# Kernel optimization log

Hardware: AMD Instinct MI355X
Metric: run time of the kernel (lower is better)

The kernel has to match this reference:

```python
import jax, jax.numpy as jnp
import numpy as np
from jax import lax

B, N, T = 64, 50, 30          # batch, history length, words per title
VOCAB, E = 50000, 300          # vocab size, word emb dim
FN, A, G, K = 400, 200, 400, 3 # filter_num, attention_dim, gru_unit, window size
USERS = 50000


def setup_inputs() -> dict:
    key = jax.random.key(0)
    ks = jax.random.split(key, 12)
    return {
        "user_id": jax.random.randint(ks[0], (B,), 0, USERS),
        "history_title": jax.random.randint(ks[1], (B, N, T), 0, VOCAB),
        "history_length": jax.random.randint(ks[2], (B,), 1, N + 1),
        "word_emb": jax.random.normal(ks[3], (VOCAB, E), jnp.float32) * 0.02,
        "conv_w": jax.random.normal(ks[4], (K, E, FN), jnp.float32) * 0.05,  # WIO layout
        "conv_b": jnp.zeros((FN,), jnp.float32),
        "v": jax.random.normal(ks[5], (FN, A), jnp.float32) * 0.05,
        "vb": jnp.zeros((A,), jnp.float32),
        "q": jax.random.normal(ks[6], (A, 1), jnp.float32) * 0.05,
        "user_emb": jax.random.normal(ks[7], (USERS, G), jnp.float32) * 0.02,
        "W_ih": jax.random.normal(ks[8], (3 * G, FN), jnp.float32) * 0.05,
        "W_hh": jax.random.normal(ks[9], (3 * G, G), jnp.float32) * 0.05,
        "b_ih": jnp.zeros((3 * G,), jnp.float32),
        "b_hh": jnp.zeros((3 * G,), jnp.float32),
    }


def _news_encode(history_title, word_emb, conv_w, conv_b, v, vb, q):
    # word embedding lookup: [B, N, T, E] (dropout is identity in eval mode)
    W = word_emb[history_title]
    # Conv1d over the word axis, padding=1 keeps length T
    x = W.reshape(B * N, T, E)
    C = lax.conv_general_dilated(
        x, conv_w, window_strides=(1,), padding=[(1, 1)],
        dimension_numbers=("NWC", "WIO", "NWC")) + conv_b
    C = jax.nn.relu(C).reshape(B, N, T, FN)
    # additive attention scores
    a = jnp.tanh(jnp.einsum("bntf,fa->bnta", C, v) + vb)
    a = jnp.einsum("bnta,ao->bnt", a, q)  # q: [A,1] -> squeeze
    # original uses Softmax(dim=0) on a [n, t] per sample => over the n-titles axis
    alpha = jax.nn.softmax(a, axis=1)
    # e[i] = alpha[i] @ C[i]: weighted sum over words -> [B, N, FN]
    return jnp.einsum("bnt,bntf->bnf", alpha, C)


def _gru(news_embed, h0, lengths, W_ih, W_hh, b_ih, b_hh):
    # packed_padded semantics: h stops updating once step >= length
    xs = jnp.swapaxes(news_embed, 0, 1)                 # [N, B, FN]
    mask = jnp.arange(N)[:, None] < lengths[None, :]    # [N, B]

    def step(h, inp):
        x_t, m = inp
        gx = x_t @ W_ih.T + b_ih                        # [B, 3G]
        gh = h @ W_hh.T + b_hh
        xr, xz, xn = jnp.split(gx, 3, axis=-1)
        hr, hz, hn = jnp.split(gh, 3, axis=-1)
        r = jax.nn.sigmoid(xr + hr)
        z = jax.nn.sigmoid(xz + hz)
        n = jnp.tanh(xn + r * hn)
        h_new = (1.0 - z) * n + z * h
        h = jnp.where(m[:, None], h_new, h)
        return h, None

    h_final, _ = lax.scan(step, h0, (xs, mask))
    return h_final


def reference(user_id, history_title, history_length, word_emb, conv_w, conv_b,
              v, vb, q, user_emb, W_ih, W_hh, b_ih, b_hh):
    news_embed = _news_encode(history_title, word_emb, conv_w, conv_b, v, vb, q)
    h0 = user_emb[user_id]                              # [B, G]
    return _gru(news_embed, h0, history_length, W_ih, W_hh, b_ih, b_hh)
```

## Files before the change

kernel.cpp:

```cpp
#include <hip/hip_runtime.h>
#include <hip/hip_bf16.h>

#define BB 64
#define NN 50
#define TT 30
#define EE 300
#define FN 400
#define AA 200
#define GG 400

typedef __attribute__((ext_vector_type(8))) short bf16x8;
typedef __attribute__((ext_vector_type(4))) float f32x4;

__global__ void k_pack_whh(const float* __restrict__ Whh, float* __restrict__ Wpack) {
  int idx = blockIdx.x * 256 + threadIdx.x;
  if (idx < 8 * 400 * 150) {
    int jl = idx % 150;
    int g = (idx / 150) % 400;
    int gc = idx / (150 * 400);
    int gate = jl / 50, gl = jl - gate * 50;
    int j = gate * 400 + gc * 50 + gl;
    Wpack[idx] = Whh[j * 400 + g];
  }
}

__global__ void k_prep_emb(const float* __restrict__ w, __hip_bfloat16* __restrict__ o) {
  long i = (long)blockIdx.x * 256 + threadIdx.x;
  if (i < (long)50000 * 320) {
    int row = (int)(i / 320), c = (int)(i % 320);
    o[i] = __float2bfloat16(c < EE ? w[(long)row * EE + c] : 0.f);
  }
}

__global__ void k_prep_wt2(const float* __restrict__ cw, __hip_bfloat16* __restrict__ o) {
  int i = blockIdx.x * 256 + threadIdx.x;
  if (i < 30 * 448 * 32) {
    int kk = i & 31, f = (i >> 5) % 448, s = i / (448 * 32);
    int ko = s / 10, e = (s - ko * 10) * 32 + kk;
    float val = (f < FN && e < EE) ? cw[(ko * EE + e) * FN + f] : 0.f;
    o[i] = __float2bfloat16(val);
  }
}

__global__ void k_prep_v(const float* __restrict__ v, __hip_bfloat16* __restrict__ o) {
  int i = blockIdx.x * 256 + threadIdx.x;
  if (i < 224 * 416) {
    int a = i / 416, f = i % 416;
    o[i] = __float2bfloat16((a < AA && f < FN) ? v[f * AA + a] : 0.f);
  }
}

__global__ void k_prep_qvb(const float* __restrict__ q, const float* __restrict__ vb,
                           float* __restrict__ qp, float* __restrict__ vbp) {
  int i = threadIdx.x;
  if (i < 224) {
    qp[i]  = i < AA ? q[i]  : 0.f;
    vbp[i] = i < AA ? vb[i] : 0.f;
  }
}

__global__ void k_prep_wih(const float* __restrict__ w, __hip_bfloat16* __restrict__ o) {
  int i = blockIdx.x * 256 + threadIdx.x;
  if (i < 1344 * 416) {
    int j = i / 416, f = i % 416;
    o[i] = __float2bfloat16((j < 1200 && f < 400) ? w[j * 400 + f] : 0.f);
  }
}

__global__ __launch_bounds__(256) void k_conv(
    const int* __restrict__ title, const __hip_bfloat16* __restrict__ emb,
    const __hip_bfloat16* __restrict__ WT2, const float* __restrict__ conv_b,
    __hip_bfloat16* __restrict__ C)
{
  __shared__ __align__(16) ushort E[2][34][328];
  __shared__ int words[60];
  const int g = blockIdx.x;
  const int tid = threadIdx.x;
  const int lane = tid & 63, wn = tid >> 6;
  const int l15 = lane & 15, l4 = lane >> 4;

  if (tid < 60) words[tid] = title[g * 60 + tid];
  __syncthreads();

  for (int idx = tid; idx < 2400; idx += 256) {
    int row = idx / 40, c = idx - row * 40;
    int ti = row / 30, w = row - ti * 30;
    const ushort* src = (const ushort*)emb + (size_t)words[row] * 320 + c * 8;
    *(uint4*)(&E[ti][w + 1][c * 8]) = *(const uint4*)src;
  }
  for (int idx = tid; idx < 320; idx += 256) {
    int z = idx / 40, c = idx - z * 40;
    int ti = z >> 2, sl = z & 3;
    int slot = (sl == 0) ? 0 : 30 + sl;
    *(uint4*)(&E[ti][slot][c * 8]) = make_uint4(0u, 0u, 0u, 0u);
  }
  __syncthreads();

  f32x4 acc[4][7];
#pragma unroll
  for (int nt = 0; nt < 7; ++nt) {
    int f = wn * 112 + nt * 16 + l15;
    float bj = (f < FN) ? conv_b[f] : 0.f;
#pragma unroll
    for (int mt = 0; mt < 4; ++mt) {
      acc[mt][nt][0] = bj; acc[mt][nt][1] = bj;
      acc[mt][nt][2] = bj; acc[mt][nt][3] = bj;
    }
  }

  const ushort* Bbase = (const ushort*)WT2 + (size_t)(wn * 112 + l15) * 32 + l4 * 8;

#pragma unroll
  for (int ko = 0; ko < 3; ++ko) {
#pragma unroll
    for (int ks = 0; ks < 10; ++ks) {
      const int s = ko * 10 + ks;
      bf16x8 bq[7];
#pragma unroll
      for (int nt = 0; nt < 7; ++nt)
        bq[nt] = *(const bf16x8*)(Bbase + (size_t)s * 14336 + nt * 512);
      bf16x8 af[4];
#pragma unroll
      for (int mt = 0; mt < 4; ++mt) {
        int row = mt * 16 + l15;
        int ti = row >> 5, slot = (row & 31) + ko;
        af[mt] = *(const bf16x8*)(&E[ti][slot][ks * 32 + l4 * 8]);
      }
#pragma unroll
      for (int nt = 0; nt < 7; ++nt)
#pragma unroll
        for (int mt = 0; mt < 4; ++mt)
          acc[mt][nt] = __builtin_amdgcn_mfma_f32_16x16x32_bf16(af[mt], bq[nt], acc[mt][nt], 0, 0, 0);
    }
  }

#pragma unroll
  for (int mt = 0; mt < 4; ++mt) {
    int rowb = mt * 16 + l4 * 4;
#pragma unroll
    for (int nt = 0; nt < 7; ++nt) {
      int f = wn * 112 + nt * 16 + l15;
      if (f < 416) {
#pragma unroll
        for (int r = 0; r < 4; ++r) {
          int row = rowb + r;
          int ti = row >> 5, t = row & 31;
          if (t < TT) {
            float vv = fmaxf(acc[mt][nt][r], 0.f);
            C[((size_t)(g * 2 + ti) * 30 + t) * 416 + f] = __float2bfloat16(vv);
          }
        }
      }
    }
  }
}

__global__ __launch_bounds__(512) void k_attn(
    const __hip_bfloat16* __restrict__ C, const __hip_bfloat16* __restrict__ vT,
    const float* __restrict__ vbp, const float* __restrict__ qp,
    float* __restrict__ score)
{
  __shared__ __align__(16) ushort Clds[256 * 40];
  __shared__ __align__(16) ushort Vlds[224 * 40];
  __shared__ float sred[2][256];
  const int tid = threadIdx.x;
  const int lane = tid & 63, wid = tid >> 6;
  const int wm = wid >> 1, wn = wid & 1;
  const int l15 = lane & 15, l4 = lane >> 4;
  const size_t row0 = (size_t)blockIdx.x * 256;

  f32x4 acc[4][7];
  float ql[7];
#pragma unroll
  for (int nt = 0; nt < 7; ++nt) {
    int a = wn * 112 + nt * 16 + l15;
    ql[nt] = qp[a];
    float vbv = vbp[a];
#pragma unroll
    for (int mt = 0; mt < 4; ++mt) {
      acc[mt][nt][0] = vbv; acc[mt][nt][1] = vbv;
      acc[mt][nt][2] = vbv; acc[mt][nt][3] = vbv;
    }
  }

  for (int ks = 0; ks < 13; ++ks) {
    for (int idx = tid; idx < 1024; idx += 512) {
      int r = idx >> 2, c = idx & 3;
      *(uint4*)(&Clds[r * 40 + c * 8]) =
          *(const uint4*)((const ushort*)C + (row0 + r) * 416 + ks * 32 + c * 8);
    }
    for (int idx = tid; idx < 896; idx += 512) {
      int a = idx >> 2, c = idx & 3;
      *(uint4*)(&Vlds[a * 40 + c * 8]) =
          *(const uint4*)((const ushort*)vT + a * 416 + ks * 32 + c * 8);
    }
    __syncthreads();
    bf16x8 cf[4];
#pragma unroll
    for (int mt = 0; mt < 4; ++mt)
      cf[mt] = *(const bf16x8*)(&Clds[(wm * 64 + mt * 16 + l15) * 40 + l4 * 8]);
#pragma unroll
    for (int nt = 0; nt < 7; ++nt) {
      bf16x8 vf = *(const bf16x8*)(&Vlds[(wn * 112 + nt * 16 + l15) * 40 + l4 * 8]);
#pragma unroll
      for (int mt = 0; mt < 4; ++mt)
        acc[mt][nt] = __builtin_amdgcn_mfma_f32_16x16x32_bf16(cf[mt], vf, acc[mt][nt], 0, 0, 0);
    }
    __syncthreads();
  }

  float sums[4][4];
#pragma unroll
  for (int mt = 0; mt < 4; ++mt)
#pragma unroll
    for (int r = 0; r < 4; ++r) sums[mt][r] = 0.f;
#pragma unroll
  for (int mt = 0; mt < 4; ++mt)
#pragma unroll
    for (int nt = 0; nt < 7; ++nt)
#pragma unroll
      for (int r = 0; r < 4; ++r)
        sums[mt][r] += tanhf(acc[mt][nt][r]) * ql[nt];
#pragma unroll
  for (int mask = 1; mask < 16; mask <<= 1)
#pragma unroll
    for (int mt = 0; mt < 4; ++mt)
#pragma unroll
      for (int r = 0; r < 4; ++r)
        sums[mt][r] += __shfl_xor(sums[mt][r], mask);

  float outv = 0.f;
#pragma unroll
  for (int mt = 0; mt < 4; ++mt)
#pragma unroll
    for (int r = 0; r < 4; ++r)
      if (l15 == mt * 4 + r) outv = sums[mt][r];
  sred[wn][wm * 64 + (l15 >> 2) * 16 + l4 * 4 + (l15 & 3)] = outv;
  __syncthreads();
  if (tid < 256) score[row0 + tid] = sred[0][tid] + sred[1][tid];
}

__global__ void k2_softmax_n(const float* __restrict__ score, float* __restrict__ alpha) {
  int i = blockIdx.x * 256 + threadIdx.x;
  if (i >= BB * TT) return;
  int b = i / TT, t = i - b * TT;
  int base = b * (NN * TT) + t;
  float m = -1e30f;
  for (int n = 0; n < NN; ++n) m = fmaxf(m, score[base + n * TT]);
  float s = 0.f;
  for (int n = 0; n < NN; ++n) s += __expf(score[base + n * TT] - m);
  float inv = 1.f / s;
  for (int n = 0; n < NN; ++n)
    alpha[base + n * TT] = __expf(score[base + n * TT] - m) * inv;
}

__global__ __launch_bounds__(256) void k3_wsum(
    const float* __restrict__ alpha, const __hip_bfloat16* __restrict__ C,
    __hip_bfloat16* __restrict__ Ebf) {
  __shared__ float al[TT];
  const int bn = blockIdx.x;
  const int tid = threadIdx.x;
  if (tid < TT) al[tid] = alpha[bn * TT + tid];
  __syncthreads();
  for (int f = tid; f < 416; f += 256) {
    float s = 0.f;
    if (f < FN) {
#pragma unroll
      for (int t = 0; t < TT; ++t)
        s = fmaf(al[t], __bfloat162float(C[((size_t)bn * TT + t) * 416 + f]), s);
    }
    Ebf[(size_t)bn * 416 + f] = __float2bfloat16(s);
  }
}

__global__ __launch_bounds__(512) void k4_gx_mfma(
    const __hip_bfloat16* __restrict__ Ebf,
    const __hip_bfloat16* __restrict__ Wih,
    const float* __restrict__ b_ih,
    float* __restrict__ gx)
{
  __shared__ __align__(16) ushort Alds[128 * 40];
  __shared__ __align__(16) ushort Blds[448 * 40];
  const int tid = threadIdx.x;
  const int lane = tid & 63, wid = tid >> 6;
  const int wm = wid >> 2, wn = wid & 3;
  const int l15 = lane & 15, l4 = lane >> 4;
  const int mb = blockIdx.x / 3;
  const int nb = blockIdx.x - mb * 3;
  const int row0 = mb * 128;
  const int n0 = nb * 448;

  f32x4 acc[4][7];
#pragma unroll
  for (int nt = 0; nt < 7; ++nt) {
    int j = n0 + wn * 112 + nt * 16 + l15;
    float bj = (j < 1200) ? b_ih[j] : 0.f;
#pragma unroll
    for (int mt = 0; mt < 4; ++mt) {
      acc[mt][nt][0] = bj; acc[mt][nt][1] = bj;
      acc[mt][nt][2] = bj; acc[mt][nt][3] = bj;
    }
  }

  const int ar = tid >> 2, ac = tid & 3;
  for (int ks = 0; ks < 13; ++ks) {
    *(uint4*)(&Alds[ar * 40 + ac * 8]) =
        *(const uint4*)((const ushort*)Ebf + (size_t)(row0 + ar) * 416 + ks * 32 + ac * 8);
    for (int idx = tid; idx < 1792; idx += 512) {
      int r = idx >> 2, c = idx & 3;
      *(uint4*)(&Blds[r * 40 + c * 8]) =
          *(const uint4*)((const ushort*)Wih + (size_t)(n0 + r) * 416 + ks * 32 + c * 8);
    }
    __syncthreads();
    bf16x8 af[4];
#pragma unroll
    for (int mt = 0; mt < 4; ++mt)
      af[mt] = *(const bf16x8*)(&Alds[(wm * 64 + mt * 16 + l15) * 40 + l4 * 8]);
#pragma unroll
    for (int nt = 0; nt < 7; ++nt) {
      bf16x8 bfr = *(const bf16x8*)(&Blds[(wn * 112 + nt * 16 + l15) * 40 + l4 * 8]);
#pragma unroll
      for (int mt = 0; mt < 4; ++mt)
        acc[mt][nt] = __builtin_amdgcn_mfma_f32_16x16x32_bf16(af[mt], bfr, acc[mt][nt], 0, 0, 0);
    }
    __syncthreads();
  }

#pragma unroll
  for (int mt = 0; mt < 4; ++mt) {
    int row = row0 + wm * 64 + mt * 16 + l4 * 4;
#pragma unroll
    for (int nt = 0; nt < 7; ++nt) {
      int j = n0 + wn * 112 + nt * 16 + l15;
      if (j < 1200) {
#pragma unroll
        for (int r = 0; r < 4; ++r)
          gx[(size_t)(row + r) * 1200 + j] = acc[mt][nt][r];
      }
    }
  }
}

__global__ void k5_init(const int* __restrict__ user_id,
                        const float* __restrict__ user_emb,
                        float* __restrict__ h0) {
  int idx = blockIdx.x * 256 + threadIdx.x;
  if (idx < BB * GG) {
    int b = idx / GG, g = idx - b * GG;
    h0[idx] = user_emb[(long)user_id[b] * GG + g];
  }
}

__global__ __launch_bounds__(256) void k5_step(
    const float* __restrict__ h_prev, float* __restrict__ h_next,
    const float* __restrict__ Wpack, const float* __restrict__ b_hh,
    const float* __restrict__ gx, const int* __restrict__ hist_len, int step)
{
  const int gc = blockIdx.x & 7;
  const int bg = blockIdx.x >> 3;
  const int tid = threadIdx.x;
  __shared__ float hl[2][GG];
  __shared__ float ghl[2][3][50];

  for (int i = tid; i < 2 * GG; i += 256) {
    int b = i / GG, g = i - b * GG;
    hl[b][g] = h_prev[(2 * bg + b) * GG + g];
  }
  __syncthreads();

  if (tid < 150) {
    float acc0 = 0.f, acc1 = 0.f;
    const float* wp = Wpack + (size_t)gc * 400 * 150 + tid;
#pragma unroll 8
    for (int g = 0; g < GG; ++g) {
      float w = wp[g * 150];
      acc0 = fmaf(hl[0][g], w, acc0);
      acc1 = fmaf(hl[1][g], w, acc1);
    }
    int gate = tid / 50, gl = tid - gate * 50;
    float bb = b_hh[gate * 400 + gc * 50 + gl];
    ghl[0][gate][gl] = acc0 + bb;
    ghl[1][gate][gl] = acc1 + bb;
  }
  __syncthreads();

  if (tid < 100) {
    int b = tid / 50, gl = tid - (tid / 50) * 50;
    int babs = 2 * bg + b;
    int g = gc * 50 + gl;
    const float* gxp = gx + ((size_t)babs * NN + step) * 1200;
    float xr = gxp[g], xz = gxp[400 + g], xn = gxp[800 + g];
    float hr = ghl[b][0][gl], hz = ghl[b][1][gl], hn = ghl[b][2][gl];
    float r = 1.f / (1.f + __expf(-(xr + hr)));
    float z = 1.f / (1.f + __expf(-(xz + hz)));
    float nv = tanhf(xn + r * hn);
    float hold = hl[b][g];
    float hnew = (1.f - z) * nv + z * hold;
    h_next[babs * GG + g] = (step < hist_len[babs]) ? hnew : hold;
  }
}

__global__ void k5_out(const float* __restrict__ h, float* __restrict__ out) {
  int idx = blockIdx.x * 256 + threadIdx.x;
  if (idx < BB * GG) out[idx] = h[idx];
}

extern "C" void kernel_launch(void* const* d_in, const int* in_sizes, int n_in,
                              void* d_out, int out_size, void* d_ws, size_t ws_size,
                              hipStream_t stream) {
  const int*   user_id   = (const int*)d_in[0];
  const int*   title     = (const int*)d_in[1];
  const int*   hist_len  = (const int*)d_in[2];
  const float* word_emb  = (const float*)d_in[3];
  const float* conv_w    = (const float*)d_in[4];
  const float* conv_b    = (const float*)d_in[5];
  const float* v         = (const float*)d_in[6];
  const float* vb        = (const float*)d_in[7];
  const float* q         = (const float*)d_in[8];
  const float* user_emb  = (const float*)d_in[9];
  const float* W_ih      = (const float*)d_in[10];
  const float* W_hh      = (const float*)d_in[11];
  const float* b_ih      = (const float*)d_in[12];
  const float* b_hh      = (const float*)d_in[13];
  float* out = (float*)d_out;

  char* ws = (char*)d_ws;
  size_t off = 0;
  auto take = [&](size_t bytes) {
    char* p = ws + off;
    off = (off + bytes + 255) & ~(size_t)255;
    return p;
  };
  __hip_bfloat16* C      = (__hip_bfloat16*)take((size_t)BB * NN * TT * 416 * 2);
  float* score  = (float*)take((size_t)BB * NN * TT * 4);
  float* alpha  = (float*)take((size_t)BB * NN * TT * 4);
  __hip_bfloat16* Ebf    = (__hip_bfloat16*)take((size_t)BB * NN * 416 * 2);
  __hip_bfloat16* Wih_bf = (__hip_bfloat16*)take((size_t)1344 * 416 * 2);
  float* Wpack  = (float*)take((size_t)8 * 400 * 150 * 4);
  float* gx     = (float*)take((size_t)BB * NN * 1200 * 4);
  float* h0     = (float*)take((size_t)BB * GG * 4);
  float* h1     = (float*)take((size_t)BB * GG * 4);
  __hip_bfloat16* emb_bf = (__hip_bfloat16*)take((size_t)50000 * 320 * 2);
  __hip_bfloat16* WT2    = (__hip_bfloat16*)take((size_t)30 * 448 * 32 * 2);
  __hip_bfloat16* vT     = (__hip_bfloat16*)take((size_t)224 * 416 * 2);
  float* qp     = (float*)take(224 * 4);
  float* vbp    = (float*)take(224 * 4);
  (void)ws_size;

  k_pack_whh<<<(8 * 400 * 150 + 255) / 256, 256, 0, stream>>>(W_hh, Wpack);
  k_prep_emb<<<(50000 * 320 + 255) / 256, 256, 0, stream>>>(word_emb, emb_bf);
  k_prep_wt2<<<(30 * 448 * 32 + 255) / 256, 256, 0, stream>>>(conv_w, WT2);
  k_prep_v<<<(224 * 416 + 255) / 256, 256, 0, stream>>>(v, vT);
  k_prep_qvb<<<1, 256, 0, stream>>>(q, vb, qp, vbp);
  k_prep_wih<<<(1344 * 416 + 255) / 256, 256, 0, stream>>>(W_ih, Wih_bf);

  k_conv<<<BB * NN / 2, 256, 0, stream>>>(title, emb_bf, WT2, conv_b, C);
  k_attn<<<BB * NN * TT / 256, 512, 0, stream>>>(C, vT, vbp, qp, score);
  k2_softmax_n<<<(BB * TT + 255) / 256, 256, 0, stream>>>(score, alpha);
  k3_wsum<<<BB * NN, 256, 0, stream>>>(alpha, C, Ebf);
  k4_gx_mfma<<<75, 512, 0, stream>>>(Ebf, Wih_bf, b_ih, gx);

  k5_init<<<(BB * GG + 255) / 256, 256, 0, stream>>>(user_id, user_emb, h0);
  float* hbuf[2] = {h0, h1};
  for (int step = 0; step < NN; ++step) {
    k5_step<<<256, 256, 0, stream>>>(hbuf[step & 1], hbuf[(step + 1) & 1],
                                     Wpack, b_hh, gx, hist_len, step);
  }
  k5_out<<<(BB * GG + 255) / 256, 256, 0, stream>>>(h0, out);
}
```

Measured before the change: 889.9 us.

## Drop full-vocab bf16 conversion, merge prep kernels, split conv per title, fuse GRU output

Removes the pass that converted the whole 50000x300 embedding table to bf16. The conv kernel now gathers fp32 rows directly and converts them in shared memory. It runs 512 threads with each set of waves handling one title, so per-wave accumulators are halved. All small weight-prep kernels and the h0 init are merged into one launch, and the final copy to the output is folded into the last GRU step. The GRU matvec is also split into two independent accumulator chains for more ILP. Gathering fp32 rows doubles the bytes read per word, but that is small next to skipping the 16M-element conversion.

```diff
diff --git a/kernel.cpp b/kernel.cpp
--- a/kernel.cpp
+++ b/kernel.cpp
@@ -12,97 +12,87 @@
 typedef __attribute__((ext_vector_type(8))) short bf16x8;
 typedef __attribute__((ext_vector_type(4))) float f32x4;
 
-__global__ void k_pack_whh(const float* __restrict__ Whh, float* __restrict__ Wpack) {
-  int idx = blockIdx.x * 256 + threadIdx.x;
-  if (idx < 8 * 400 * 150) {
-    int jl = idx % 150;
-    int g = (idx / 150) % 400;
-    int gc = idx / (150 * 400);
+__device__ inline ushort f2bf(float x) {
+  __hip_bfloat16 b = __float2bfloat16(x);
+  return *(ushort*)&b;
+}
+
+__global__ void k_prep_all(
+    const float* __restrict__ Whh, const float* __restrict__ cw,
+    const float* __restrict__ v, const float* __restrict__ q,
+    const float* __restrict__ vb, const float* __restrict__ Wih,
+    const int* __restrict__ user_id, const float* __restrict__ user_emb,
+    float* __restrict__ Wpack, __hip_bfloat16* __restrict__ WT2,
+    __hip_bfloat16* __restrict__ vT, float* __restrict__ qp,
+    float* __restrict__ vbp, __hip_bfloat16* __restrict__ Wih_bf,
+    float* __restrict__ h0)
+{
+  int i = blockIdx.x * 256 + threadIdx.x;
+  if (i < 480000) {
+    int jl = i % 150;
+    int g = (i / 150) % 400;
+    int gc = i / 60000;
     int gate = jl / 50, gl = jl - gate * 50;
     int j = gate * 400 + gc * 50 + gl;
-    Wpack[idx] = Whh[j * 400 + g];
-  }
-}
-
-__global__ void k_prep_emb(const float* __restrict__ w, __hip_bfloat16* __restrict__ o) {
-  long i = (long)blockIdx.x * 256 + threadIdx.x;
-  if (i < (long)50000 * 320) {
-    int row = (int)(i / 320), c = (int)(i % 320);
-    o[i] = __float2bfloat16(c < EE ? w[(long)row * EE + c] : 0.f);
-  }
-}
-
-__global__ void k_prep_wt2(const float* __restrict__ cw, __hip_bfloat16* __restrict__ o) {
-  int i = blockIdx.x * 256 + threadIdx.x;
-  if (i < 30 * 448 * 32) {
-    int kk = i & 31, f = (i >> 5) % 448, s = i / (448 * 32);
+    Wpack[i] = Whh[j * 400 + g];
+  } else if (i < 910080) {
+    int k = i - 480000;
+    int kk = k & 31, f = (k >> 5) % 448, s = k / (448 * 32);
     int ko = s / 10, e = (s - ko * 10) * 32 + kk;
     float val = (f < FN && e < EE) ? cw[(ko * EE + e) * FN + f] : 0.f;
-    o[i] = __float2bfloat16(val);
-  }
-}
-
-__global__ void k_prep_v(const float* __restrict__ v, __hip_bfloat16* __restrict__ o) {
-  int i = blockIdx.x * 256 + threadIdx.x;
-  if (i < 224 * 416) {
-    int a = i / 416, f = i % 416;
-    o[i] = __float2bfloat16((a < AA && f < FN) ? v[f * AA + a] : 0.f);
-  }
-}
-
-__global__ void k_prep_qvb(const float* __restrict__ q, const float* __restrict__ vb,
-                           float* __restrict__ qp, float* __restrict__ vbp) {
-  int i = threadIdx.x;
-  if (i < 224) {
-    qp[i]  = i < AA ? q[i]  : 0.f;
-    vbp[i] = i < AA ? vb[i] : 0.f;
-  }
-}
-
-__global__ void k_prep_wih(const float* __restrict__ w, __hip_bfloat16* __restrict__ o) {
-  int i = blockIdx.x * 256 + threadIdx.x;
-  if (i < 1344 * 416) {
-    int j = i / 416, f = i % 416;
-    o[i] = __float2bfloat16((j < 1200 && f < 400) ? w[j * 400 + f] : 0.f);
-  }
-}
-
-__global__ __launch_bounds__(256) void k_conv(
-    const int* __restrict__ title, const __hip_bfloat16* __restrict__ emb,
+    WT2[k] = __float2bfloat16(val);
+  } else if (i < 1003264) {
+    int k = i - 910080;
+    int a = k / 416, f = k % 416;
+    vT[k] = __float2bfloat16((a < AA && f < FN) ? v[f * AA + a] : 0.f);
+  } else if (i < 1003488) {
+    int k = i - 1003264;
+    qp[k]  = k < AA ? q[k]  : 0.f;
+    vbp[k] = k < AA ? vb[k] : 0.f;
+  } else if (i < 1562592) {
+    int k = i - 1003488;
+    int j = k / 416, f = k % 416;
+    Wih_bf[k] = __float2bfloat16((j < 1200 && f < FN) ? Wih[j * 400 + f] : 0.f);
+  } else if (i < 1588192) {
+    int k = i - 1562592;
+    int b = k / GG, g = k - b * GG;
+    h0[k] = user_emb[(size_t)user_id[b] * GG + g];
+  }
+}
+
+__global__ __launch_bounds__(512, 4) void k_conv(
+    const int* __restrict__ title, const float* __restrict__ word_emb,
     const __hip_bfloat16* __restrict__ WT2, const float* __restrict__ conv_b,
     __hip_bfloat16* __restrict__ C)
 {
-  __shared__ __align__(16) ushort E[2][34][328];
+  __shared__ __align__(16) ushort E[2][34][340];
   __shared__ int words[60];
   const int g = blockIdx.x;
   const int tid = threadIdx.x;
-  const int lane = tid & 63, wn = tid >> 6;
+  const int lane = tid & 63, wid = tid >> 6;
+  const int ti = wid >> 2, wn = wid & 3;
   const int l15 = lane & 15, l4 = lane >> 4;
 
   if (tid < 60) words[tid] = title[g * 60 + tid];
-  __syncthreads();
-
-  for (int idx = tid; idx < 2400; idx += 256) {
-    int row = idx / 40, c = idx - row * 40;
-    int ti = row / 30, w = row - ti * 30;
-    const ushort* src = (const ushort*)emb + (size_t)words[row] * 320 + c * 8;
-    *(uint4*)(&E[ti][w + 1][c * 8]) = *(const uint4*)src;
-  }
-  for (int idx = tid; idx < 320; idx += 256) {
-    int z = idx / 40, c = idx - z * 40;
-    int ti = z >> 2, sl = z & 3;
-    int slot = (sl == 0) ? 0 : 30 + sl;
-    *(uint4*)(&E[ti][slot][c * 8]) = make_uint4(0u, 0u, 0u, 0u);
-  }
-  __syncthreads();
-
-  f32x4 acc[4][7];
+  for (int idx = tid; idx < 2890; idx += 512)
+    *(uint4*)((ushort*)E + idx * 8) = make_uint4(0u, 0u, 0u, 0u);
+  __syncthreads();
+  for (int idx = tid; idx < 4500; idx += 512) {
+    int row = idx / 75, ch = idx - row * 75;
+    int tt = row / 30, w = row - tt * 30;
+    float4 v4 = *(const float4*)(word_emb + (size_t)words[row] * EE + ch * 4);
+    ushort4 u4 = make_ushort4(f2bf(v4.x), f2bf(v4.y), f2bf(v4.z), f2bf(v4.w));
+    *(ushort4*)(&E[tt][w + 1][ch * 4]) = u4;
+  }
+  __syncthreads();
+
+  f32x4 acc[2][7];
 #pragma unroll
   for (int nt = 0; nt < 7; ++nt) {
     int f = wn * 112 + nt * 16 + l15;
     float bj = (f < FN) ? conv_b[f] : 0.f;
 #pragma unroll
-    for (int mt = 0; mt < 4; ++mt) {
+    for (int mt = 0; mt < 2; ++mt) {
       acc[mt][nt][0] = bj; acc[mt][nt][1] = bj;
       acc[mt][nt][2] = bj; acc[mt][nt][3] = bj;
     }
@@ -119,32 +109,28 @@
 #pragma unroll
       for (int nt = 0; nt < 7; ++nt)
         bq[nt] = *(const bf16x8*)(Bbase + (size_t)s * 14336 + nt * 512);
-      bf16x8 af[4];
-#pragma unroll
-      for (int mt = 0; mt < 4; ++mt) {
-        int row = mt * 16 + l15;
-        int ti = row >> 5, slot = (row & 31) + ko;
-        af[mt] = *(const bf16x8*)(&E[ti][slot][ks * 32 + l4 * 8]);
-      }
+      bf16x8 af[2];
+#pragma unroll
+      for (int mt = 0; mt < 2; ++mt)
+        af[mt] = *(const bf16x8*)(&E[ti][mt * 16 + l15 + ko][ks * 32 + l4 * 8]);
 #pragma unroll
       for (int nt = 0; nt < 7; ++nt)
 #pragma unroll
-        for (int mt = 0; mt < 4; ++mt)
+        for (int mt = 0; mt < 2; ++mt)
           acc[mt][nt] = __builtin_amdgcn_mfma_f32_16x16x32_bf16(af[mt], bq[nt], acc[mt][nt], 0, 0, 0);
     }
   }
 
 #pragma unroll
-  for (int mt = 0; mt < 4; ++mt) {
-    int rowb = mt * 16 + l4 * 4;
+  for (int mt = 0; mt < 2; ++mt) {
+    int tb = mt * 16 + l4 * 4;
 #pragma unroll
     for (int nt = 0; nt < 7; ++nt) {
       int f = wn * 112 + nt * 16 + l15;
       if (f < 416) {
 #pragma unroll
         for (int r = 0; r < 4; ++r) {
-          int row = rowb + r;
-          int ti = row >> 5, t = row & 31;
+          int t = tb + r;
           if (t < TT) {
             float vv = fmaxf(acc[mt][nt][r], 0.f);
             C[((size_t)(g * 2 + ti) * 30 + t) * 416 + f] = __float2bfloat16(vv);
@@ -341,20 +327,11 @@
   }
 }
 
-__global__ void k5_init(const int* __restrict__ user_id,
-                        const float* __restrict__ user_emb,
-                        float* __restrict__ h0) {
-  int idx = blockIdx.x * 256 + threadIdx.x;
-  if (idx < BB * GG) {
-    int b = idx / GG, g = idx - b * GG;
-    h0[idx] = user_emb[(long)user_id[b] * GG + g];
-  }
-}
-
 __global__ __launch_bounds__(256) void k5_step(
     const float* __restrict__ h_prev, float* __restrict__ h_next,
     const float* __restrict__ Wpack, const float* __restrict__ b_hh,
-    const float* __restrict__ gx, const int* __restrict__ hist_len, int step)
+    const float* __restrict__ gx, const int* __restrict__ hist_len,
+    float* __restrict__ out, int step)
 {
   const int gc = blockIdx.x & 7;
   const int bg = blockIdx.x >> 3;
@@ -369,18 +346,21 @@
   __syncthreads();
 
   if (tid < 150) {
-    float acc0 = 0.f, acc1 = 0.f;
-    const float* wp = Wpack + (size_t)gc * 400 * 150 + tid;
-#pragma unroll 8
-    for (int g = 0; g < GG; ++g) {
-      float w = wp[g * 150];
-      acc0 = fmaf(hl[0][g], w, acc0);
-      acc1 = fmaf(hl[1][g], w, acc1);
+    float a00 = 0.f, a01 = 0.f, a10 = 0.f, a11 = 0.f;
+    const float* wp = Wpack + (size_t)gc * 60000 + tid;
+#pragma unroll 4
+    for (int g = 0; g < 200; ++g) {
+      float w0 = wp[g * 150];
+      float w1 = wp[(g + 200) * 150];
+      a00 = fmaf(hl[0][g], w0, a00);
+      a10 = fmaf(hl[1][g], w0, a10);
+      a01 = fmaf(hl[0][g + 200], w1, a01);
+      a11 = fmaf(hl[1][g + 200], w1, a11);
     }
     int gate = tid / 50, gl = tid - gate * 50;
     float bb = b_hh[gate * 400 + gc * 50 + gl];
-    ghl[0][gate][gl] = acc0 + bb;
-    ghl[1][gate][gl] = acc1 + bb;
+    ghl[0][gate][gl] = a00 + a01 + bb;
+    ghl[1][gate][gl] = a10 + a11 + bb;
   }
   __syncthreads();
 
@@ -396,13 +376,10 @@
     float nv = tanhf(xn + r * hn);
     float hold = hl[b][g];
     float hnew = (1.f - z) * nv + z * hold;
-    h_next[babs * GG + g] = (step < hist_len[babs]) ? hnew : hold;
-  }
-}
-
-__global__ void k5_out(const float* __restrict__ h, float* __restrict__ out) {
-  int idx = blockIdx.x * 256 + threadIdx.x;
-  if (idx < BB * GG) out[idx] = h[idx];
+    float hres = (step < hist_len[babs]) ? hnew : hold;
+    h_next[babs * GG + g] = hres;
+    if (step == NN - 1) out[babs * GG + g] = hres;
+  }
 }
 
 extern "C" void kernel_launch(void* const* d_in, const int* in_sizes, int n_in,
@@ -440,31 +417,25 @@
   float* gx     = (float*)take((size_t)BB * NN * 1200 * 4);
   float* h0     = (float*)take((size_t)BB * GG * 4);
   float* h1     = (float*)take((size_t)BB * GG * 4);
-  __hip_bfloat16* emb_bf = (__hip_bfloat16*)take((size_t)50000 * 320 * 2);
   __hip_bfloat16* WT2    = (__hip_bfloat16*)take((size_t)30 * 448 * 32 * 2);
   __hip_bfloat16* vT     = (__hip_bfloat16*)take((size_t)224 * 416 * 2);
   float* qp     = (float*)take(224 * 4);
   float* vbp    = (float*)take(224 * 4);
   (void)ws_size;
 
-  k_pack_whh<<<(8 * 400 * 150 + 255) / 256, 256, 0, stream>>>(W_hh, Wpack);
-  k_prep_emb<<<(50000 * 320 + 255) / 256, 256, 0, stream>>>(word_emb, emb_bf);
-  k_prep_wt2<<<(30 * 448 * 32 + 255) / 256, 256, 0, stream>>>(conv_w, WT2);
-  k_prep_v<<<(224 * 416 + 255) / 256, 256, 0, stream>>>(v, vT);
-  k_prep_qvb<<<1, 256, 0, stream>>>(q, vb, qp, vbp);
-  k_prep_wih<<<(1344 * 416 + 255) / 256, 256, 0, stream>>>(W_ih, Wih_bf);
-
-  k_conv<<<BB * NN / 2, 256, 0, stream>>>(title, emb_bf, WT2, conv_b, C);
+  k_prep_all<<<6204, 256, 0, stream>>>(W_hh, conv_w, v, q, vb, W_ih, user_id,
+                                       user_emb, Wpack, WT2, vT, qp, vbp,
+                                       Wih_bf, h0);
+
+  k_conv<<<BB * NN / 2, 512, 0, stream>>>(title, word_emb, WT2, conv_b, C);
   k_attn<<<BB * NN * TT / 256, 512, 0, stream>>>(C, vT, vbp, qp, score);
   k2_softmax_n<<<(BB * TT + 255) / 256, 256, 0, stream>>>(score, alpha);
   k3_wsum<<<BB * NN, 256, 0, stream>>>(alpha, C, Ebf);
   k4_gx_mfma<<<75, 512, 0, stream>>>(Ebf, Wih_bf, b_ih, gx);
 
-  k5_init<<<(BB * GG + 255) / 256, 256, 0, stream>>>(user_id, user_emb, h0);
   float* hbuf[2] = {h0, h1};
   for (int step = 0; step < NN; ++step) {
     k5_step<<<256, 256, 0, stream>>>(hbuf[step & 1], hbuf[(step + 1) & 1],
-                                     Wpack, b_hh, gx, hist_len, step);
-  }
-  k5_out<<<(BB * GG + 255) / 256, 256, 0, stream>>>(h0, out);
-}
+                                     Wpack, b_hh, gx, hist_len, out, step);
+  }
+}
```

After: 894.5 us. No clear change (+0.5%).
